# Kernel tuning notes

Hardware: AMD Instinct MI355X
Metric: run time of the kernel (lower is better)

The kernel has to match this reference:

```python
import jax, jax.numpy as jnp
import numpy as np

N = 40000
C_IN, C_OUT = 64, 128
SHAPE = (512, 16, 512)   # (x, height, z); dim=1 -> n_kernels=16
BEV_H, BEV_W = 512, 512  # bev_dims = [0, 2]
N_KERNELS = 16
BATCH = 2


def setup_inputs() -> dict:
    key = jax.random.key(0)
    k1, k2, k3, k4, k5, k6 = jax.random.split(key, 6)
    x = jax.random.randint(k1, (N,), 0, BEV_H, dtype=jnp.int32)
    h = jax.random.randint(k2, (N,), 0, N_KERNELS, dtype=jnp.int32)
    z = jax.random.randint(k3, (N,), 0, BEV_W, dtype=jnp.int32)
    b = jax.random.randint(k4, (N,), 0, BATCH, dtype=jnp.int32)
    coords = jnp.stack([x, h, z, b], axis=1)  # [N, 4]
    feats = jax.random.normal(k5, (N, C_IN), dtype=jnp.float32)
    std = 1.0 / np.sqrt(C_IN)
    kernel = jax.random.uniform(k6, (N_KERNELS, C_IN, C_OUT), dtype=jnp.float32,
                                minval=-std, maxval=std)
    return {"coords": coords, "feats": feats, "kernel": kernel,
            "stride": 1, "batch_size": BATCH}


def reference(coords, feats, kernel, stride, batch_size):
    # gather per-point kernel by height bin (dim=1), offset is zero
    kidx = coords[:, 1] // stride                      # [N]
    per_point_k = kernel[kidx]                         # [N, C_in, C_out]
    f = jnp.einsum('nc,nco->no', feats, per_point_k)   # [N, C_out]
    # flat BEV index: batch * (H*W) + x * W + z
    b = coords[:, 3].astype(jnp.int32)
    xb = (coords[:, 0] // stride).astype(jnp.int32)
    zb = (coords[:, 2] // stride).astype(jnp.int32)
    idx = b * (BEV_H * BEV_W) + xb * BEV_W + zb        # [N]
    num_seg = batch_size * BEV_H * BEV_W
    dense = jax.ops.segment_sum(f, idx, num_segments=num_seg)  # [B*H*W, C_out]
    out = dense.reshape(batch_size, BEV_H, BEV_W, C_OUT)
    return jnp.transpose(out, (0, 3, 1, 2))            # [B, C_out, H, W]
```

## Files before the change

### kernel.cpp

```cpp
#include <hip/hip_runtime.h>


#define CIN   64
#define COUT  128
#define BEVH  512
#define BEVW  512
#define HW    (BEVH * BEVW)

__global__ __launch_bounds__(256) void bev_point(
    const int*   __restrict__ coords,
    const float* __restrict__ feats,
    const float* __restrict__ kern,
    const int*   __restrict__ stride_p,
    float*       __restrict__ f,
    int*         __restrict__ head,
    int*         __restrict__ nxt,
    unsigned int* __restrict__ bm,
    int n)
{
    const int wave = threadIdx.x >> 6;
    const int lane = threadIdx.x & 63;
    int pt = blockIdx.x * 4 + wave;
    if (pt >= n) return;
    pt = __builtin_amdgcn_readfirstlane(pt);

    const int stride = stride_p[0];
    const int cx = coords[pt * 4 + 0];
    const int ch = coords[pt * 4 + 1];
    const int cz = coords[pt * 4 + 2];
    const int cb = coords[pt * 4 + 3];

    const int k  = ch / stride;
    const int xb = cx / stride;
    const int zb = cz / stride;

    const float* fp = feats + (size_t)pt * CIN;
    const float* kp = kern + (size_t)k * (CIN * COUT) + 2 * lane;

    float ax = 0.f, ay = 0.f;
#pragma unroll
    for (int c = 0; c < CIN; ++c) {
        const float fv = fp[c];
        const float2 kv = *(const float2*)(kp + c * COUT);
        ax = fmaf(fv, kv.x, ax);
        ay = fmaf(fv, kv.y, ay);
    }

    *(float2*)(f + (size_t)pt * COUT + 2 * lane) = make_float2(ax, ay);

    if (lane == 0) {
        const int cell = cb * HW + xb * BEVW + zb;
        const int old = atomicExch(&head[cell], pt);
        nxt[pt] = old;
        atomicOr(&bm[cell >> 5], 1u << (cell & 31));
    }
}

__global__ __launch_bounds__(256) void bev_dense(
    const float*        __restrict__ f,
    const int*          __restrict__ head,
    const int*          __restrict__ nxt,
    const unsigned int* __restrict__ bm,
    float*              __restrict__ out,
    int total4)
{
    const int t = blockIdx.x * 256 + threadIdx.x;
    if (t >= total4) return;
    const int linear = t << 2;
    const int z = linear & 511;
    const int x = (linear >> 9) & 511;
    const int o = (linear >> 18) & 127;
    const int b = linear >> 25;
    const int cell = (b << 18) + (x << 9) + z;

    const unsigned int word = bm[cell >> 5];
    const unsigned int nib  = (word >> (cell & 31)) & 0xFu;

    float4 v = make_float4(0.f, 0.f, 0.f, 0.f);
    if (nib) {
        float acc[4] = {0.f, 0.f, 0.f, 0.f};
#pragma unroll
        for (int j = 0; j < 4; ++j) {
            if (nib & (1u << j)) {
                int p = head[cell + j];
                while (p >= 0) {
                    acc[j] += f[(size_t)p * COUT + o];
                    p = nxt[p];
                }
            }
        }
        v = make_float4(acc[0], acc[1], acc[2], acc[3]);
    }
    *(float4*)(out + linear) = v;
}

extern "C" void kernel_launch(void* const* d_in, const int* in_sizes, int n_in,
                              void* d_out, int out_size, void* d_ws, size_t ws_size,
                              hipStream_t stream) {
    const int*   coords   = (const int*)d_in[0];
    const float* feats    = (const float*)d_in[1];
    const float* kern     = (const float*)d_in[2];
    const int*   stride_p = (const int*)d_in[3];
    float* out = (float*)d_out;

    const int n      = in_sizes[0] / 4;
    const int ncells = out_size / COUT;

    size_t off = 0;
    float* f = (float*)((char*)d_ws + off);      off += (size_t)n * COUT * sizeof(float);
    int* head = (int*)((char*)d_ws + off);       off += (size_t)ncells * sizeof(int);
    int* nxt  = (int*)((char*)d_ws + off);       off += (size_t)n * sizeof(int);
    unsigned int* bm = (unsigned int*)((char*)d_ws + off); off += (size_t)(ncells / 8);

    if (ws_size >= off) {
        hipMemsetAsync(head, 0xFF, (size_t)ncells * sizeof(int), stream);
        hipMemsetAsync(bm, 0, (size_t)(ncells / 8), stream);

        bev_point<<<(n + 3) / 4, 256, 0, stream>>>(coords, feats, kern, stride_p,
                                                   f, head, nxt, bm, n);
        const int total4 = out_size / 4;
        bev_dense<<<(total4 + 255) / 256, 256, 0, stream>>>(f, head, nxt, bm, out, total4);
    } else {
        hipMemsetAsync(d_out, 0, (size_t)out_size * sizeof(float), stream);
        bev_point<<<1, 1, 0, stream>>>(coords, feats, kern, stride_p,
                                       (float*)d_ws, (int*)d_ws, (int*)d_ws,
                                       (unsigned int*)d_ws, 0);
    }
}
```

Measured before the change: 399.9 us.

## Bucket points by height bin and reuse LDS-staged kernel across point batches

Adds a counting-sort pass that groups point indices by kernel bin. The point kernel then stages one bin's 64x128 weight matrix in LDS and has each wave process 8 points, so weight loads are reused instead of being re-read from global memory for every point. The dense kernel now writes four tiles per thread, and the workspace-size fallback is removed. The costs are an extra launch, a sorted buffer of size 16*n, and a point-kernel grid with many blocks that exit early.

Measured after the change: 397.0 us. About the same (-0.7%).

```diff
diff --git a/kernel.cpp b/kernel.cpp
--- a/kernel.cpp
+++ b/kernel.cpp
@@ -1,58 +1,119 @@
 #include <hip/hip_runtime.h>
 
 
-#define CIN   64
-#define COUT  128
-#define BEVH  512
-#define BEVW  512
-#define HW    (BEVH * BEVW)
+#define CIN    64
+#define COUT   128
+#define BEVH   512
+#define BEVW   512
+#define HW     (BEVH * BEVW)
+#define NBINS  16
+#define PTS_PER_WAVE  8
+#define PTS_PER_BLOCK 32
+
+__global__ __launch_bounds__(256) void bev_sort(
+    const int* __restrict__ coords,
+    const int* __restrict__ stride_p,
+    int*       __restrict__ gcnt,
+    int*       __restrict__ sorted,
+    int n)
+{
+    __shared__ int hist[NBINS];
+    __shared__ int base[NBINS];
+    const int tid = threadIdx.x;
+    if (tid < NBINS) hist[tid] = 0;
+    __syncthreads();
+
+    const int i = blockIdx.x * 256 + tid;
+    int k = 0, rank = 0;
+    if (i < n) {
+        k = coords[i * 4 + 1] / stride_p[0];
+        rank = atomicAdd(&hist[k], 1);
+    }
+    __syncthreads();
+    if (tid < NBINS)
+        base[tid] = hist[tid] ? atomicAdd(&gcnt[tid], hist[tid]) : 0;
+    __syncthreads();
+    if (i < n)
+        sorted[k * n + base[k] + rank] = i;
+}
 
 __global__ __launch_bounds__(256) void bev_point(
     const int*   __restrict__ coords,
     const float* __restrict__ feats,
     const float* __restrict__ kern,
     const int*   __restrict__ stride_p,
+    const int*   __restrict__ gcnt,
+    const int*   __restrict__ sorted,
     float*       __restrict__ f,
     int*         __restrict__ head,
     int*         __restrict__ nxt,
     unsigned int* __restrict__ bm,
-    int n)
+    int n, int chunks_per_bin)
 {
+    __shared__ float lk[CIN * COUT];
+
+    const int bin   = blockIdx.x / chunks_per_bin;
+    const int chunk = blockIdx.x % chunks_per_bin;
+    const int cnt   = gcnt[bin];
+    const int r0blk = chunk * PTS_PER_BLOCK;
+    if (r0blk >= cnt) return;
+
+    {
+        const float4* src = (const float4*)(kern + (size_t)bin * CIN * COUT);
+        float4* dst = (float4*)lk;
+#pragma unroll
+        for (int j = 0; j < 8; ++j)
+            dst[j * 256 + threadIdx.x] = src[j * 256 + threadIdx.x];
+    }
+    __syncthreads();
+
     const int wave = threadIdx.x >> 6;
     const int lane = threadIdx.x & 63;
-    int pt = blockIdx.x * 4 + wave;
-    if (pt >= n) return;
-    pt = __builtin_amdgcn_readfirstlane(pt);
+    const int r0 = r0blk + wave * PTS_PER_WAVE;
+    const int navail = cnt - r0;
+    if (navail <= 0) return;
+    const int np = navail < PTS_PER_WAVE ? navail : PTS_PER_WAVE;
 
-    const int stride = stride_p[0];
-    const int cx = coords[pt * 4 + 0];
-    const int ch = coords[pt * 4 + 1];
-    const int cz = coords[pt * 4 + 2];
-    const int cb = coords[pt * 4 + 3];
+    int pts[PTS_PER_WAVE];
+#pragma unroll
+    for (int p = 0; p < PTS_PER_WAVE; ++p) {
+        const int rr = (p < np) ? (r0 + p) : r0;
+        pts[p] = __builtin_amdgcn_readfirstlane(sorted[bin * n + rr]);
+    }
 
-    const int k  = ch / stride;
-    const int xb = cx / stride;
-    const int zb = cz / stride;
+    float ax[PTS_PER_WAVE], ay[PTS_PER_WAVE];
+#pragma unroll
+    for (int p = 0; p < PTS_PER_WAVE; ++p) { ax[p] = 0.f; ay[p] = 0.f; }
 
-    const float* fp = feats + (size_t)pt * CIN;
-    const float* kp = kern + (size_t)k * (CIN * COUT) + 2 * lane;
-
-    float ax = 0.f, ay = 0.f;
 #pragma unroll
     for (int c = 0; c < CIN; ++c) {
-        const float fv = fp[c];
-        const float2 kv = *(const float2*)(kp + c * COUT);
-        ax = fmaf(fv, kv.x, ax);
-        ay = fmaf(fv, kv.y, ay);
+        const float2 kv = *(const float2*)&lk[c * COUT + 2 * lane];
+#pragma unroll
+        for (int p = 0; p < PTS_PER_WAVE; ++p) {
+            const float fv = feats[(size_t)pts[p] * CIN + c];
+            ax[p] = fmaf(fv, kv.x, ax[p]);
+            ay[p] = fmaf(fv, kv.y, ay[p]);
+        }
     }
 
-    *(float2*)(f + (size_t)pt * COUT + 2 * lane) = make_float2(ax, ay);
+#pragma unroll
+    for (int p = 0; p < PTS_PER_WAVE; ++p) {
+        if (p < np)
+            *(float2*)(f + (size_t)pts[p] * COUT + 2 * lane) = make_float2(ax[p], ay[p]);
+    }
 
     if (lane == 0) {
-        const int cell = cb * HW + xb * BEVW + zb;
-        const int old = atomicExch(&head[cell], pt);
-        nxt[pt] = old;
-        atomicOr(&bm[cell >> 5], 1u << (cell & 31));
+        const int stride = stride_p[0];
+        for (int p = 0; p < np; ++p) {
+            const int pt = pts[p];
+            const int cx = coords[pt * 4 + 0];
+            const int cz = coords[pt * 4 + 2];
+            const int cb = coords[pt * 4 + 3];
+            const int cell = cb * HW + (cx / stride) * BEVW + (cz / stride);
+            const int old = atomicExch(&head[cell], pt);
+            nxt[pt] = old;
+            atomicOr(&bm[cell >> 5], 1u << (cell & 31));
+        }
     }
 }
 
@@ -62,36 +123,39 @@
     const int*          __restrict__ nxt,
     const unsigned int* __restrict__ bm,
     float*              __restrict__ out,
-    int total4)
+    int quarter4)
 {
     const int t = blockIdx.x * 256 + threadIdx.x;
-    if (t >= total4) return;
-    const int linear = t << 2;
-    const int z = linear & 511;
-    const int x = (linear >> 9) & 511;
-    const int o = (linear >> 18) & 127;
-    const int b = linear >> 25;
-    const int cell = (b << 18) + (x << 9) + z;
+    if (t >= quarter4) return;
 
-    const unsigned int word = bm[cell >> 5];
-    const unsigned int nib  = (word >> (cell & 31)) & 0xFu;
+#pragma unroll
+    for (int r = 0; r < 4; ++r) {
+        const int tile   = t + r * quarter4;
+        const int linear = tile << 2;
+        const int z = linear & 511;
+        const int x = (linear >> 9) & 511;
+        const int o = (linear >> 18) & 127;
+        const int b = linear >> 25;
+        const int cell = (b << 18) + (x << 9) + z;
 
-    float4 v = make_float4(0.f, 0.f, 0.f, 0.f);
-    if (nib) {
-        float acc[4] = {0.f, 0.f, 0.f, 0.f};
+        const unsigned int nib = (bm[cell >> 5] >> (cell & 31)) & 0xFu;
+        float4 v = make_float4(0.f, 0.f, 0.f, 0.f);
+        if (nib) {
+            float acc[4] = {0.f, 0.f, 0.f, 0.f};
 #pragma unroll
-        for (int j = 0; j < 4; ++j) {
-            if (nib & (1u << j)) {
-                int p = head[cell + j];
-                while (p >= 0) {
-                    acc[j] += f[(size_t)p * COUT + o];
-                    p = nxt[p];
+            for (int j = 0; j < 4; ++j) {
+                if (nib & (1u << j)) {
+                    int p = head[cell + j];
+                    while (p >= 0) {
+                        acc[j] += f[(size_t)p * COUT + o];
+                        p = nxt[p];
+                    }
                 }
             }
+            v = make_float4(acc[0], acc[1], acc[2], acc[3]);
         }
-        v = make_float4(acc[0], acc[1], acc[2], acc[3]);
+        *(float4*)(out + linear) = v;
     }
-    *(float4*)(out + linear) = v;
 }
 
 extern "C" void kernel_launch(void* const* d_in, const int* in_sizes, int n_in,
@@ -107,23 +171,22 @@
     const int ncells = out_size / COUT;
 
     size_t off = 0;
-    float* f = (float*)((char*)d_ws + off);      off += (size_t)n * COUT * sizeof(float);
-    int* head = (int*)((char*)d_ws + off);       off += (size_t)ncells * sizeof(int);
-    int* nxt  = (int*)((char*)d_ws + off);       off += (size_t)n * sizeof(int);
+    float* f = (float*)((char*)d_ws + off);          off += (size_t)n * COUT * sizeof(float);
+    int* head = (int*)((char*)d_ws + off);           off += (size_t)ncells * sizeof(int);
+    int* nxt  = (int*)((char*)d_ws + off);           off += (size_t)n * sizeof(int);
+    int* sorted = (int*)((char*)d_ws + off);         off += (size_t)NBINS * n * sizeof(int);
     unsigned int* bm = (unsigned int*)((char*)d_ws + off); off += (size_t)(ncells / 8);
+    int* gcnt = (int*)((char*)d_ws + off);           off += NBINS * sizeof(int);
 
-    if (ws_size >= off) {
-        hipMemsetAsync(head, 0xFF, (size_t)ncells * sizeof(int), stream);
-        hipMemsetAsync(bm, 0, (size_t)(ncells / 8), stream);
+    hipMemsetAsync(head, 0xFF, (size_t)ncells * sizeof(int), stream);
+    hipMemsetAsync(bm, 0, (size_t)(ncells / 8) + NBINS * sizeof(int), stream);
 
-        bev_point<<<(n + 3) / 4, 256, 0, stream>>>(coords, feats, kern, stride_p,
-                                                   f, head, nxt, bm, n);
-        const int total4 = out_size / 4;
-        bev_dense<<<(total4 + 255) / 256, 256, 0, stream>>>(f, head, nxt, bm, out, total4);
-    } else {
-        hipMemsetAsync(d_out, 0, (size_t)out_size * sizeof(float), stream);
-        bev_point<<<1, 1, 0, stream>>>(coords, feats, kern, stride_p,
-                                       (float*)d_ws, (int*)d_ws, (int*)d_ws,
-                                       (unsigned int*)d_ws, 0);
-    }
+    bev_sort<<<(n + 255) / 256, 256, 0, stream>>>(coords, stride_p, gcnt, sorted, n);
+
+    const int chunks_per_bin = (n + PTS_PER_BLOCK - 1) / PTS_PER_BLOCK;
+    bev_point<<<NBINS * chunks_per_bin, 256, 0, stream>>>(
+        coords, feats, kern, stride_p, gcnt, sorted, f, head, nxt, bm, n, chunks_per_bin);
+
+    const int quarter4 = out_size / 16;
+    bev_dense<<<(quarter4 + 255) / 256, 256, 0, stream>>>(f, head, nxt, bm, out, quarter4);
 }
```
